# Kernel tuning notes

Measured on AMD Instinct MI355X. Metric: run time of the kernel, lower is better.

## Reference

```python
import jax, jax.numpy as jnp
import numpy as np
from jax import lax

NEG = jnp.float32(-1e9)
POS = jnp.float32(1e9)


def _edt_sq(mask):
    """Exact squared Euclidean distance transform of a 2D boolean mask.

    mask: [H, W] bool, True = foreground (nonzero in scipy terms).
    Returns [H, W] float32 squared distance to nearest background (False) pixel.
    Felzenszwalb-Huttenlocher separable formulation:
      pass 1 (axis 0): 1D distance to nearest zero per column (O(H) via scans)
      pass 2 (axis 1): min-plus convolution with quadratic per row.
    """
    H, W = mask.shape
    zero = ~mask
    idx = jnp.broadcast_to(jnp.arange(H, dtype=jnp.float32)[:, None], (H, W))
    # index of last background pixel at-or-above, and next at-or-below, per column
    last0 = lax.associative_scan(jnp.maximum, jnp.where(zero, idx, NEG), axis=0)
    next0 = jnp.flip(
        lax.associative_scan(jnp.minimum, jnp.flip(jnp.where(zero, idx, POS), 0), axis=0), 0)
    d1 = jnp.minimum(idx - last0, next0 - idx)  # 1D distance along axis 0
    f = jnp.where(mask, d1 * d1, jnp.float32(0.0))  # squared axis-0 distance
    # pass 2: D[i, j] = min_j' f[i, j'] + (j - j')^2
    jq = jnp.arange(W, dtype=jnp.float32)
    q = (jq[:, None] - jq[None, :]) ** 2  # [W, W]
    def row_min(frow):  # frow: [W]
        return jnp.min(frow[None, :] + q, axis=1)  # [W]
    return lax.map(row_min, f)  # [H, W]


def setup_inputs() -> dict:
    key = jax.random.key(0)
    img = jax.random.uniform(key, (2048, 2048), dtype=jnp.float32)
    return {"img": img}


def reference(img) -> jnp.ndarray:
    mask = img > 0.5  # scipy: nonzero pixels are foreground
    d = jnp.sqrt(_edt_sq(mask))
    m = jnp.max(d)
    d = jnp.where(m > 0, d / m * 255.0, d)  # `if img.max() != 0: img = img/max*255`
    return d.astype(jnp.uint8)  # img.astype(np.uint8)
```

## Files before the change

kernel.cpp:

```cpp
#include <hip/hip_runtime.h>
#include <math.h>

typedef unsigned long long u64;

#define H 2048
#define W 2048
#define NWR 64
#define TILE 128
#define HALO 32
#define LW (TILE + 2 * HALO)
#define DCLAMP 2900
#define NTHR 256

__device__ __forceinline__ int vfar_up(const unsigned* __restrict__ rmask, int col, int r, int ks) {
    for (int kk = ks - 2; kk >= 0; --kk) {
        unsigned w = rmask[kk * W + col];
        if (w) return r - (kk * 32 + (31 - __clz(w)));
    }
    return DCLAMP;
}
__device__ __forceinline__ int vfar_dn(const unsigned* __restrict__ rmask, int col, int r, int ks) {
    for (int kk = ks + 2; kk < NWR; ++kk) {
        unsigned w = rmask[kk * W + col];
        if (w) return (kk * 32 + (__ffs(w) - 1)) - r;
    }
    return DCLAMP;
}

__device__ float f_from_mask(const unsigned* __restrict__ rmask, int col, int r) {
    int kw = r >> 5, b = r & 31;
    unsigned wm1 = (kw > 0)       ? rmask[(kw - 1) * W + col] : 0u;
    unsigned w0  =                  rmask[kw * W + col];
    unsigned wp1 = (kw < NWR - 1) ? rmask[(kw + 1) * W + col] : 0u;
    if ((w0 >> b) & 1u) return 0.0f;
    u64 A  = (u64)wm1 | ((u64)w0 << 32);
    u64 Bv = (u64)w0  | ((u64)wp1 << 32);
    int p = 32 + b;
    u64 Am = A & ((1ull << p) - 1ull);
    int da = Am ? (p - (63 - __clzll(Am))) : vfar_up(rmask, col, r, kw);
    u64 Bm = Bv >> (b + 1);
    int db = Bm ? __ffsll(Bm) : vfar_dn(rmask, col, r, kw);
    int d1 = min(min(da, db), DCLAMP);
    return (float)d1 * (float)d1;
}

__global__ void k1_pack(const float* __restrict__ img, unsigned* __restrict__ rmask,
                        unsigned int* __restrict__ maxp) {
    int gid = blockIdx.x * NTHR + threadIdx.x;
    if (gid == 0) *maxp = 0u;
    int col = gid & (W - 1);
    int kw  = gid >> 11;
    unsigned w = 0;
#pragma unroll
    for (int i = 0; i < 32; ++i)
        w |= (img[(size_t)(kw * 32 + i) * W + col] <= 0.5f ? 1u : 0u) << i;
    rmask[kw * W + col] = w;
}

__global__ void __launch_bounds__(NTHR)
k2_edt(const unsigned* __restrict__ rmask, float* __restrict__ dist,
       unsigned int* __restrict__ maxp) {
    __shared__ float ftile[32][LW];
    __shared__ float smax[4];
    const int tid = threadIdx.x;
    const int c0 = blockIdx.x * TILE;
    const int ks = blockIdx.y;
    const int rbase = ks * 32;

    if (tid < LW) {
        int gc = c0 - HALO + tid;
        if (gc >= 0 && gc < W) {
            unsigned wm1 = (ks > 0)       ? rmask[(ks - 1) * W + gc] : 0u;
            unsigned w0  =                  rmask[ks * W + gc];
            unsigned wp1 = (ks < NWR - 1) ? rmask[(ks + 1) * W + gc] : 0u;
            u64 A  = (u64)wm1 | ((u64)w0 << 32);
            u64 Bv = (u64)w0  | ((u64)wp1 << 32);
#pragma unroll
            for (int i = 0; i < 32; ++i) {
                int p = 32 + i;
                u64 Am = A & ((1ull << p) - 1ull);
                int da = Am ? (p - (63 - __clzll(Am))) : vfar_up(rmask, gc, rbase + i, ks);
                u64 Bm = Bv >> (i + 1);
                int db = Bm ? __ffsll(Bm) : vfar_dn(rmask, gc, rbase + i, ks);
                int d1 = min(min(da, db), DCLAMP);
                float fd = (float)d1;
                ftile[i][tid] = ((w0 >> i) & 1u) ? 0.0f : fd * fd;
            }
        } else {
#pragma unroll
            for (int i = 0; i < 32; ++i)
                ftile[i][tid] = 1e9f;
        }
    }
    __syncthreads();

    const int col = tid & (TILE - 1);
    const int rh  = tid >> 7;
    const int lj  = HALO + col;
    const int jj  = c0 + col;
    float res[16];
    float lmax = 0.0f;
#pragma unroll 2
    for (int t = 0; t < 16; ++t) {
        const int i = rh * 16 + t;
        float best = ftile[i][lj];
#pragma unroll
        for (int d = 1; d <= 8; ++d) {
            float q = (float)(d * d);
            best = fminf(best, ftile[i][lj - d] + q);
            best = fminf(best, ftile[i][lj + d] + q);
        }
        if (81.0f < best) {
            for (int d = 9; d <= HALO && (float)(d * d) < best; ++d) {
                float q = (float)(d * d);
                best = fminf(best, ftile[i][lj - d] + q);
                best = fminf(best, ftile[i][lj + d] + q);
            }
            if ((float)((HALO + 1) * (HALO + 1)) < best) {
                int r = rbase + i;
                for (int d = HALO + 1; d < W && (float)(d * d) < best; ++d) {
                    float q = (float)(d * d);
                    int jm = jj - d, jp = jj + d;
                    if (jm >= 0) best = fminf(best, f_from_mask(rmask, jm, r) + q);
                    if (jp < W)  best = fminf(best, f_from_mask(rmask, jp, r) + q);
                }
            }
        }
        float rr = sqrtf(best);
        res[t] = rr;
        lmax = fmaxf(lmax, rr);
    }
#pragma unroll
    for (int t = 0; t < 16; ++t)
        dist[(size_t)(rbase + rh * 16 + t) * W + jj] = res[t];

    for (int o = 32; o > 0; o >>= 1) lmax = fmaxf(lmax, __shfl_down(lmax, o, 64));
    if ((tid & 63) == 0) smax[tid >> 6] = lmax;
    __syncthreads();
    if (tid == 0)
        atomicMax(maxp, __float_as_uint(fmaxf(fmaxf(smax[0], smax[1]),
                                              fmaxf(smax[2], smax[3]))));
}

__global__ void k3_norm(int* __restrict__ out, const unsigned int* __restrict__ maxp) {
    size_t idx = ((size_t)blockIdx.x * NTHR + threadIdx.x) * 4;
    float m = __uint_as_float(*maxp);
    float4 dv = *(const float4*)((const float*)out + idx);
    float r[4] = {dv.x, dv.y, dv.z, dv.w};
    int o[4];
#pragma unroll
    for (int k = 0; k < 4; ++k) {
        float v = (m > 0.0f) ? (r[k] / m * 255.0f) : r[k];
        v = fminf(fmaxf(v, 0.0f), 255.0f);
        o[k] = (int)v;
    }
    *(int4*)(out + idx) = make_int4(o[0], o[1], o[2], o[3]);
}

extern "C" void kernel_launch(void* const* d_in, const int* in_sizes, int n_in,
                              void* d_out, int out_size, void* d_ws, size_t ws_size,
                              hipStream_t stream) {
    const float* img = (const float*)d_in[0];
    int* out = (int*)d_out;

    unsigned* rmask = (unsigned*)d_ws;
    unsigned int* maxp = (unsigned int*)((char*)d_ws + (size_t)NWR * W * 4);

    k1_pack<<<dim3(NWR * W / NTHR), dim3(NTHR), 0, stream>>>(img, rmask, maxp);
    k2_edt <<<dim3(W / TILE, NWR), dim3(NTHR), 0, stream>>>(rmask, (float*)out, maxp);
    k3_norm<<<dim3(H * W / (NTHR * 4)), dim3(NTHR), 0, stream>>>(out, maxp);
}
```

Before: 93.82 us.

## Register-block EDT row pass and stage output through LDS for float4 stores

Remaps k2 threads so each thread handles one row and 16 consecutive columns, preloading a 32-wide window of the squared column distances into registers. The common radius-8 min-plus search then runs from registers instead of repeated shared-memory reads. The shared tile is padded to a stride of 193 to avoid bank conflicts. Results are written back through LDS so global stores become coalesced float4 writes. The rare far-search helpers are marked noinline to keep register pressure down, at the cost of the extra 32-float register array and the additional barriers.

New measurement: 91.07 us. -2.9%, faster.

```diff
diff --git a/kernel.cpp b/kernel.cpp
--- a/kernel.cpp
+++ b/kernel.cpp
@@ -8,18 +8,19 @@
 #define NWR 64
 #define TILE 128
 #define HALO 32
-#define LW (TILE + 2 * HALO)
+#define LW 192
+#define LSTRIDE 193
 #define DCLAMP 2900
 #define NTHR 256
 
-__device__ __forceinline__ int vfar_up(const unsigned* __restrict__ rmask, int col, int r, int ks) {
+__device__ __attribute__((noinline)) int vfar_up(const unsigned* rmask, int col, int r, int ks) {
     for (int kk = ks - 2; kk >= 0; --kk) {
         unsigned w = rmask[kk * W + col];
         if (w) return r - (kk * 32 + (31 - __clz(w)));
     }
     return DCLAMP;
 }
-__device__ __forceinline__ int vfar_dn(const unsigned* __restrict__ rmask, int col, int r, int ks) {
+__device__ __attribute__((noinline)) int vfar_dn(const unsigned* rmask, int col, int r, int ks) {
     for (int kk = ks + 2; kk < NWR; ++kk) {
         unsigned w = rmask[kk * W + col];
         if (w) return (kk * 32 + (__ffs(w) - 1)) - r;
@@ -27,7 +28,7 @@
     return DCLAMP;
 }
 
-__device__ float f_from_mask(const unsigned* __restrict__ rmask, int col, int r) {
+__device__ __attribute__((noinline)) float f_from_mask(const unsigned* rmask, int col, int r) {
     int kw = r >> 5, b = r & 31;
     unsigned wm1 = (kw > 0)       ? rmask[(kw - 1) * W + col] : 0u;
     unsigned w0  =                  rmask[kw * W + col];
@@ -60,7 +61,7 @@
 __global__ void __launch_bounds__(NTHR)
 k2_edt(const unsigned* __restrict__ rmask, float* __restrict__ dist,
        unsigned int* __restrict__ maxp) {
-    __shared__ float ftile[32][LW];
+    __shared__ float ftile[32][LSTRIDE];
     __shared__ float smax[4];
     const int tid = threadIdx.x;
     const int c0 = blockIdx.x * TILE;
@@ -94,30 +95,33 @@
     }
     __syncthreads();
 
-    const int col = tid & (TILE - 1);
-    const int rh  = tid >> 7;
-    const int lj  = HALO + col;
-    const int jj  = c0 + col;
+    const int i  = tid & 31;
+    const int p  = tid >> 5;
+    const int lc = HALO + p * 16;
+    float reg[32];
+#pragma unroll
+    for (int k = 0; k < 32; ++k)
+        reg[k] = ftile[i][lc - 8 + k];
+
     float res[16];
     float lmax = 0.0f;
-#pragma unroll 2
-    for (int t = 0; t < 16; ++t) {
-        const int i = rh * 16 + t;
-        float best = ftile[i][lj];
+#pragma unroll
+    for (int m = 0; m < 16; ++m) {
+        float best = reg[m + 8];
 #pragma unroll
         for (int d = 1; d <= 8; ++d) {
             float q = (float)(d * d);
-            best = fminf(best, ftile[i][lj - d] + q);
-            best = fminf(best, ftile[i][lj + d] + q);
+            best = fminf(best, reg[m + 8 - d] + q);
+            best = fminf(best, reg[m + 8 + d] + q);
         }
-        if (81.0f < best) {
+        if (__builtin_expect(81.0f < best, 0)) {
             for (int d = 9; d <= HALO && (float)(d * d) < best; ++d) {
                 float q = (float)(d * d);
-                best = fminf(best, ftile[i][lj - d] + q);
-                best = fminf(best, ftile[i][lj + d] + q);
+                best = fminf(best, ftile[i][lc + m - d] + q);
+                best = fminf(best, ftile[i][lc + m + d] + q);
             }
             if ((float)((HALO + 1) * (HALO + 1)) < best) {
-                int r = rbase + i;
+                int r = rbase + i, jj = c0 + p * 16 + m;
                 for (int d = HALO + 1; d < W && (float)(d * d) < best; ++d) {
                     float q = (float)(d * d);
                     int jm = jj - d, jp = jj + d;
@@ -127,12 +131,23 @@
             }
         }
         float rr = sqrtf(best);
-        res[t] = rr;
+        res[m] = rr;
         lmax = fmaxf(lmax, rr);
     }
+
+    __syncthreads();
 #pragma unroll
-    for (int t = 0; t < 16; ++t)
-        dist[(size_t)(rbase + rh * 16 + t) * W + jj] = res[t];
+    for (int m = 0; m < 16; ++m)
+        ftile[i][p * 16 + m] = res[m];
+    __syncthreads();
+#pragma unroll
+    for (int q = 0; q < 4; ++q) {
+        int r  = (tid >> 5) + 8 * q;
+        int c4 = (tid & 31) * 4;
+        float4 v = make_float4(ftile[r][c4], ftile[r][c4 + 1],
+                               ftile[r][c4 + 2], ftile[r][c4 + 3]);
+        *(float4*)(dist + (size_t)(rbase + r) * W + c0 + c4) = v;
+    }
 
     for (int o = 32; o > 0; o >>= 1) lmax = fmaxf(lmax, __shfl_down(lmax, o, 64));
     if ((tid & 63) == 0) smax[tid >> 6] = lmax;
```
